# Kernel tuning notes

Hardware: AMD Instinct MI355X
Metric: run time of the kernel (lower is better)

## Reference

```python
import jax, jax.numpy as jnp
import numpy as np

ALPHA = 1.0  # set_privacy(True)


def setup_inputs() -> dict:
    key = jax.random.key(0)
    k1, k2, k3, k4, k5, k6 = jax.random.split(key, 6)
    B, S, IN, OUT = 2, 1024, 4096, 11008
    NNZ = 2250000
    x = jax.random.normal(k1, (B, S, IN), dtype=jnp.float32)
    scales = jax.random.uniform(k2, (OUT,), dtype=jnp.float32)  # positive per-row scales
    ortho_vals = jax.random.normal(k3, (NNZ,), dtype=jnp.float32)
    base_packed = jax.random.randint(k4, (OUT, IN // 2), 0, 256, dtype=jnp.int32)
    ortho_rows = jnp.sort(jax.random.randint(k5, (NNZ,), 0, OUT, dtype=jnp.int32))
    ortho_cols = jax.random.randint(k6, (NNZ,), 0, IN, dtype=jnp.int32)
    return {"x": x, "scales": scales, "ortho_vals": ortho_vals,
            "base_packed": base_packed, "ortho_rows": ortho_rows, "ortho_cols": ortho_cols}


def _dequant_weight(base_packed, scales):
    OUT, HALF = base_packed.shape
    low = base_packed & 0xF          # packed column 2j  -> original column 2j
    high = (base_packed >> 4) & 0xF  # packed column 2j  -> original column 2j+1
    # interleave low/high nibbles back to [OUT, IN]
    w_off = jnp.stack([low, high], axis=-1).reshape(OUT, 2 * HALF)
    return (w_off.astype(jnp.float32) - 8.0) * scales[:, None]


def reference(x, scales, ortho_vals, base_packed, ortho_rows, ortho_cols):
    OUT = base_packed.shape[0]
    IN = base_packed.shape[1] * 2
    w_base = _dequant_weight(base_packed, scales)  # [OUT, IN] fp32
    w_sparse = jnp.zeros((OUT, IN), dtype=jnp.float32).at[ortho_rows, ortho_cols].add(
        ortho_vals.astype(jnp.float32))
    w = w_base + ALPHA * w_sparse
    x_flat = x.reshape(-1, IN).astype(jnp.float32)
    out = x_flat @ w.T  # [tokens, OUT]
    return out.reshape(x.shape[:-1] + (OUT,)).astype(x.dtype)
```

## Files before the change

kernel.cpp:

```cpp
#include <hip/hip_runtime.h>
#include <stdint.h>

#define ALPHA 1.0f

typedef int i32x4 __attribute__((ext_vector_type(4)));

typedef __attribute__((address_space(3))) void lds_void_t;
typedef const __attribute__((address_space(1))) void global_void_t;

__device__ __forceinline__ void async16(const void* g, void* l) {
    __builtin_amdgcn_global_load_lds((global_void_t*)g, (lds_void_t*)l, 16, 0, 0);
}

__device__ __forceinline__ signed char q8(float v, float inv) {
    float f = fminf(fmaxf(v * inv, -127.f), 127.f);
    return (signed char)__float2int_rn(f);
}

__global__ __launch_bounds__(256) void prep_kernel(
    const float* __restrict__ x, const int* __restrict__ rows,
    int* __restrict__ rstart, int* __restrict__ rend,
    signed char* __restrict__ X8, float* __restrict__ sx, int M, int nnz) {
    const int b = blockIdx.x;
    if (b < M) {
        __shared__ float red[4];
        const int t = threadIdx.x;
        const float4* xr = (const float4*)(x + (size_t)b * 4096);
        float4 v[4];
        float mx = 0.f;
#pragma unroll
        for (int i = 0; i < 4; i++) {
            v[i] = xr[t * 4 + i];
            mx = fmaxf(mx, fmaxf(fmaxf(fabsf(v[i].x), fabsf(v[i].y)),
                                 fmaxf(fabsf(v[i].z), fabsf(v[i].w))));
        }
#pragma unroll
        for (int o = 32; o > 0; o >>= 1) mx = fmaxf(mx, __shfl_xor(mx, o));
        if ((t & 63) == 0) red[t >> 6] = mx;
        __syncthreads();
        mx = fmaxf(fmaxf(red[0], red[1]), fmaxf(red[2], red[3]));
        mx = fmaxf(mx, 1e-20f);
        if (t == 0) sx[b] = mx / 127.f;
        const float inv = 127.f / mx;
        union { signed char c[16]; int4 w; } u;
#pragma unroll
        for (int i = 0; i < 4; i++) {
            u.c[i * 4 + 0] = q8(v[i].x, inv);
            u.c[i * 4 + 1] = q8(v[i].y, inv);
            u.c[i * 4 + 2] = q8(v[i].z, inv);
            u.c[i * 4 + 3] = q8(v[i].w, inv);
        }
        ((int4*)(X8 + (size_t)b * 4096))[t] = u.w;
    } else {
        int i = (b - M) * 256 + threadIdx.x;
        if (i < nnz) {
            int r = rows[i];
            if (i == 0 || rows[i - 1] != r) rstart[r] = i;
            if (i == nnz - 1 || rows[i + 1] != r) rend[r] = i + 1;
        }
    }
}

__global__ __launch_bounds__(256) void build_w8_kernel(
    const int* __restrict__ packed, const float* __restrict__ scales,
    const float* __restrict__ vals, const int* __restrict__ cols,
    const int* __restrict__ rstart, const int* __restrict__ rend,
    signed char* __restrict__ W8, float* __restrict__ sw) {
    __shared__ float acc[4096];
    __shared__ float red[4];
    const int r = blockIdx.x;
    const int t = threadIdx.x;
    const int4* prow = (const int4*)(packed + (size_t)r * 2048);
    const float s = scales[r];

    int4 p0 = prow[t], p1 = prow[t + 256];
#pragma unroll
    for (int h = 0; h < 2; h++) {
        int4 p = h ? p1 : p0;
        int base = 8 * (t + 256 * h);
        int pv[4] = {p.x, p.y, p.z, p.w};
#pragma unroll
        for (int q = 0; q < 4; q++) {
            acc[base + 2 * q]     = (float)((pv[q] & 0xF) - 8) * s;
            acc[base + 2 * q + 1] = (float)(((pv[q] >> 4) & 0xF) - 8) * s;
        }
    }
    __syncthreads();

    const int lo = rstart[r], hi = rend[r];
    for (int i = lo + t; i < hi; i += 256)
        atomicAdd(&acc[cols[i]], vals[i] * ALPHA);
    __syncthreads();

    float4 f[4];
    float mx = 0.f;
#pragma unroll
    for (int i = 0; i < 4; i++) {
        f[i] = ((const float4*)acc)[t * 4 + i];
        mx = fmaxf(mx, fmaxf(fmaxf(fabsf(f[i].x), fabsf(f[i].y)),
                             fmaxf(fabsf(f[i].z), fabsf(f[i].w))));
    }
#pragma unroll
    for (int o = 32; o > 0; o >>= 1) mx = fmaxf(mx, __shfl_xor(mx, o));
    if ((t & 63) == 0) red[t >> 6] = mx;
    __syncthreads();
    mx = fmaxf(fmaxf(red[0], red[1]), fmaxf(red[2], red[3]));
    mx = fmaxf(mx, 1e-20f);
    if (t == 0) sw[r] = mx / 127.f;
    const float inv = 127.f / mx;

    union { signed char c[16]; int4 w; } u;
#pragma unroll
    for (int i = 0; i < 4; i++) {
        u.c[i * 4 + 0] = q8(f[i].x, inv);
        u.c[i * 4 + 1] = q8(f[i].y, inv);
        u.c[i * 4 + 2] = q8(f[i].z, inv);
        u.c[i * 4 + 3] = q8(f[i].w, inv);
    }
    ((int4*)(W8 + (size_t)r * 4096))[t] = u.w;
}

__global__ __launch_bounds__(512) void gemm_kernel(
    const signed char* __restrict__ Xq,
    const signed char* __restrict__ Wq,
    const float* __restrict__ sx,
    const float* __restrict__ sw,
    float* __restrict__ C,
    int M, int N, int K) {
    __shared__ __align__(16) signed char smem[3 * 49152];

    const int tid  = threadIdx.x;
    const int wid  = tid >> 6;
    const int lane = tid & 63;
    const int wr = wid >> 2;
    const int wc = wid & 3;

    const int nwg = gridDim.x;
    const int bid = blockIdx.x;
    const int qc = nwg >> 3, rr = nwg & 7;
    const int xcd = bid & 7, loc = bid >> 3;
    const int swz = (xcd < rr ? xcd * (qc + 1) : rr * (qc + 1) + (xcd - rr) * qc) + loc;
    const int tm = M >> 7;
    const int mt = swz % tm;
    const int nt = swz / tm;
    const int m0 = mt << 7;
    const int n0 = nt << 8;

    const int sr = tid >> 3;
    const int sc = ((tid & 7) ^ (sr & 7)) << 4;
    const int lw0 = wid << 10;
    const int lw1 = 8192 + (wid << 10);

    const signed char* Ax  = Xq + (size_t)m0 * K;
    const signed char* Bw0 = Wq + (size_t)n0 * K;
    const signed char* Bw1 = Wq + (size_t)(n0 + 128) * K;

#define STAGE(gbase, ldsbase) do {                                         \
        async16((gbase) + (size_t)sr * K + sc, (ldsbase) + lw0);           \
        async16((gbase) + (size_t)(sr + 64) * K + sc, (ldsbase) + lw1);    \
    } while (0)

    const int fm = lane & 15;
    const int slot0 = ((lane >> 4) ^ (lane & 7)) << 4;
    const int slot1 = slot0 ^ 64;
    const int arow_base = wr * 64;
    const int brow_base = wc * 64;

#define LDA(buf, mi, sl) \
    (*(const i32x4*)((buf) + (size_t)(arow_base + (mi) * 16 + fm) * 128 + (sl)))
#define LDB(buf, nj, sl) \
    (*(const i32x4*)((buf) + 16384 + (size_t)(brow_base + (nj) * 16 + fm) * 128 + (sl)))

#define MFMA8(m0i, m1i, aX, aY, B0, B1, B2, B3) do {                        \
        __builtin_amdgcn_s_setprio(1);                                      \
        acc[m0i][0] = __builtin_amdgcn_mfma_i32_16x16x64_i8(aX, B0, acc[m0i][0], 0, 0, 0); \
        acc[m1i][0] = __builtin_amdgcn_mfma_i32_16x16x64_i8(aY, B0, acc[m1i][0], 0, 0, 0); \
        acc[m0i][1] = __builtin_amdgcn_mfma_i32_16x16x64_i8(aX, B1, acc[m0i][1], 0, 0, 0); \
        acc[m1i][1] = __builtin_amdgcn_mfma_i32_16x16x64_i8(aY, B1, acc[m1i][1], 0, 0, 0); \
        acc[m0i][2] = __builtin_amdgcn_mfma_i32_16x16x64_i8(aX, B2, acc[m0i][2], 0, 0, 0); \
        acc[m1i][2] = __builtin_amdgcn_mfma_i32_16x16x64_i8(aY, B2, acc[m1i][2], 0, 0, 0); \
        acc[m0i][3] = __builtin_amdgcn_mfma_i32_16x16x64_i8(aX, B3, acc[m0i][3], 0, 0, 0); \
        acc[m1i][3] = __builtin_amdgcn_mfma_i32_16x16x64_i8(aY, B3, acc[m1i][3], 0, 0, 0); \
        __builtin_amdgcn_s_setprio(0);                                      \
    } while (0)

    i32x4 acc[4][4];
#pragma unroll
    for (int i = 0; i < 4; i++)
#pragma unroll
        for (int j = 0; j < 4; j++) acc[i][j] = (i32x4){0, 0, 0, 0};

    const int NT = K >> 7;

    STAGE(Ax,        smem);
    STAGE(Bw0,       smem + 16384);
    STAGE(Bw1,       smem + 32768);
    STAGE(Ax  + 128, smem + 49152);
    STAGE(Bw0 + 128, smem + 49152 + 16384);
    STAGE(Bw1 + 128, smem + 49152 + 32768);
    asm volatile("s_waitcnt vmcnt(6)" ::: "memory");
    __builtin_amdgcn_s_barrier();
    __builtin_amdgcn_sched_barrier(0);

    int cur = 0;
    for (int it = 0; it < NT; ++it) {
        signed char* Ab = smem + cur * 49152;
        int pb = cur + 2; if (pb >= 3) pb -= 3;
        signed char* PA = smem + pb * 49152;
        const bool pref = (it + 2 < NT);
        const int kc = (it + 2) << 7;

        i32x4 a0  = LDA(Ab, 0, slot0), a1  = LDA(Ab, 1, slot0);
        i32x4 bA0 = LDB(Ab, 0, slot0), bA1 = LDB(Ab, 1, slot0),
              bA2 = LDB(Ab, 2, slot0), bA3 = LDB(Ab, 3, slot0);
        i32x4 na0 = LDA(Ab, 2, slot0), na1 = LDA(Ab, 3, slot0);
        if (pref) STAGE(Ax + kc, PA);
        MFMA8(0, 1, a0, a1, bA0, bA1, bA2, bA3);

        i32x4 bB0 = LDB(Ab, 0, slot1), bB1 = LDB(Ab, 1, slot1),
              bB2 = LDB(Ab, 2, slot1), bB3 = LDB(Ab, 3, slot1);
        i32x4 ma0 = LDA(Ab, 0, slot1), ma1 = LDA(Ab, 1, slot1);
        if (pref) STAGE(Bw0 + kc, PA + 16384);
        MFMA8(2, 3, na0, na1, bA0, bA1, bA2, bA3);

        i32x4 pa2 = LDA(Ab, 2, slot1), pa3 = LDA(Ab, 3, slot1);
        if (pref) STAGE(Bw1 + kc, PA + 32768);
        MFMA8(0, 1, ma0, ma1, bB0, bB1, bB2, bB3);

        if (it + 2 < NT)       { asm volatile("s_waitcnt vmcnt(6)" ::: "memory"); }
        else if (it + 2 == NT) { asm volatile("s_waitcnt vmcnt(0)" ::: "memory"); }
        MFMA8(2, 3, pa2, pa3, bB0, bB1, bB2, bB3);

        __builtin_amdgcn_s_barrier();
        __builtin_amdgcn_sched_barrier(0);
        cur += 1; if (cur == 3) cur = 0;
    }
#undef STAGE
#undef LDA
#undef LDB
#undef MFMA8

    const int cr = (lane >> 4) << 2;
    const int cc = lane & 15;
#pragma unroll
    for (int mi = 0; mi < 4; ++mi) {
        const int row0 = m0 + wr * 64 + mi * 16 + cr;
        float sxv[4];
#pragma unroll
        for (int r = 0; r < 4; ++r) sxv[r] = sx[row0 + r];
#pragma unroll
        for (int nj = 0; nj < 4; ++nj) {
            const int col = n0 + wc * 64 + nj * 16 + cc;
            const float swc = sw[col];
            float* cp = C + (size_t)row0 * N + col;
#pragma unroll
            for (int r = 0; r < 4; ++r)
                cp[(size_t)r * N] = (float)acc[mi][nj][r] * sxv[r] * swc;
        }
    }
}

extern "C" void kernel_launch(void* const* d_in, const int* in_sizes, int n_in,
                              void* d_out, int out_size, void* d_ws, size_t ws_size,
                              hipStream_t stream) {
    const float* x      = (const float*)d_in[0];
    const float* scales = (const float*)d_in[1];
    const float* vals   = (const float*)d_in[2];
    const int* packed   = (const int*)d_in[3];
    const int* rows     = (const int*)d_in[4];
    const int* cols     = (const int*)d_in[5];
    float* out          = (float*)d_out;

    const int OUT  = in_sizes[1];
    const int HALF = in_sizes[3] / OUT;
    const int IN   = HALF * 2;
    const int M    = in_sizes[0] / IN;
    const int NNZ  = in_sizes[2];

    signed char* W8 = (signed char*)d_ws;
    signed char* X8 = W8 + (size_t)OUT * IN;
    float* sx   = (float*)(X8 + (size_t)M * IN);
    float* sw   = sx + M;
    int* rstart = (int*)(sw + OUT);
    int* rend   = rstart + OUT;

    const int boundsBlocks = (NNZ + 255) / 256;
    prep_kernel<<<M + boundsBlocks, 256, 0, stream>>>(x, rows, rstart, rend,
                                                      X8, sx, M, NNZ);
    build_w8_kernel<<<OUT, 256, 0, stream>>>(packed, scales, vals, cols,
                                             rstart, rend, W8, sw);
    const int nwg = (M / 128) * (OUT / 256);
    gemm_kernel<<<nwg, 512, 0, stream>>>(X8, W8, sx, sw, out, M, OUT, IN);
}
```

Before: 314.0 us.

## Shrink GEMM tile to 128x128 with 256 threads and double-buffered LDS

Reworks the int8 GEMM from a 128x256 tile with 8 waves and a triple-buffered LDS pipeline (prefetch two ahead) into a 128x128 tile with 4 waves and a double-buffered pipeline (prefetch one ahead). Launch bounds now request two blocks per CU, and the smaller LDS footprint makes that possible, so the aim is more occupancy and latency hiding across blocks. In exchange there is less operand reuse per tile, the grid doubles, and each iteration waits on vmcnt(0) before its barrier, which may expose global load latency. OUT=11008 divides by 128 evenly, so coverage is preserved.

```diff
diff --git a/kernel.cpp b/kernel.cpp
--- a/kernel.cpp
+++ b/kernel.cpp
@@ -120,20 +120,20 @@
     ((int4*)(W8 + (size_t)r * 4096))[t] = u.w;
 }
 
-__global__ __launch_bounds__(512) void gemm_kernel(
+__global__ __launch_bounds__(256, 2) void gemm_kernel(
     const signed char* __restrict__ Xq,
     const signed char* __restrict__ Wq,
     const float* __restrict__ sx,
     const float* __restrict__ sw,
     float* __restrict__ C,
     int M, int N, int K) {
-    __shared__ __align__(16) signed char smem[3 * 49152];
+    __shared__ __align__(16) signed char smem[2 * 32768];
 
     const int tid  = threadIdx.x;
     const int wid  = tid >> 6;
     const int lane = tid & 63;
-    const int wr = wid >> 2;
-    const int wc = wid & 3;
+    const int wr = wid >> 1;
+    const int wc = wid & 1;
 
     const int nwg = gridDim.x;
     const int bid = blockIdx.x;
@@ -144,20 +144,23 @@
     const int mt = swz % tm;
     const int nt = swz / tm;
     const int m0 = mt << 7;
-    const int n0 = nt << 8;
+    const int n0 = nt << 7;
 
     const int sr = tid >> 3;
     const int sc = ((tid & 7) ^ (sr & 7)) << 4;
-    const int lw0 = wid << 10;
-    const int lw1 = 8192 + (wid << 10);
-
-    const signed char* Ax  = Xq + (size_t)m0 * K;
-    const signed char* Bw0 = Wq + (size_t)n0 * K;
-    const signed char* Bw1 = Wq + (size_t)(n0 + 128) * K;
-
-#define STAGE(gbase, ldsbase) do {                                         \
-        async16((gbase) + (size_t)sr * K + sc, (ldsbase) + lw0);           \
-        async16((gbase) + (size_t)(sr + 64) * K + sc, (ldsbase) + lw1);    \
+    const int lw = wid << 10;
+
+    const signed char* Ax = Xq + (size_t)m0 * K;
+    const signed char* Bw = Wq + (size_t)n0 * K;
+
+#define STAGE(abase, bbase, ldsbase) do {                                    \
+        _Pragma("unroll")                                                    \
+        for (int i_ = 0; i_ < 4; i_++) {                                     \
+            async16((abase) + (size_t)(i_ * 32 + sr) * K + sc,               \
+                    (ldsbase) + i_ * 4096 + lw);                             \
+            async16((bbase) + (size_t)(i_ * 32 + sr) * K + sc,               \
+                    (ldsbase) + 16384 + i_ * 4096 + lw);                     \
+        }                                                                    \
     } while (0)
 
     const int fm = lane & 15;
@@ -192,48 +195,35 @@
 
     const int NT = K >> 7;
 
-    STAGE(Ax,        smem);
-    STAGE(Bw0,       smem + 16384);
-    STAGE(Bw1,       smem + 32768);
-    STAGE(Ax  + 128, smem + 49152);
-    STAGE(Bw0 + 128, smem + 49152 + 16384);
-    STAGE(Bw1 + 128, smem + 49152 + 32768);
-    asm volatile("s_waitcnt vmcnt(6)" ::: "memory");
+    STAGE(Ax, Bw, smem);
+    asm volatile("s_waitcnt vmcnt(0)" ::: "memory");
     __builtin_amdgcn_s_barrier();
     __builtin_amdgcn_sched_barrier(0);
 
-    int cur = 0;
     for (int it = 0; it < NT; ++it) {
-        signed char* Ab = smem + cur * 49152;
-        int pb = cur + 2; if (pb >= 3) pb -= 3;
-        signed char* PA = smem + pb * 49152;
-        const bool pref = (it + 2 < NT);
-        const int kc = (it + 2) << 7;
+        signed char* Ab = smem + ((it & 1) << 15);
+        signed char* Pb = smem + (((it + 1) & 1) << 15);
+        const int kc = (it + 1) << 7;
 
         i32x4 a0  = LDA(Ab, 0, slot0), a1  = LDA(Ab, 1, slot0);
         i32x4 bA0 = LDB(Ab, 0, slot0), bA1 = LDB(Ab, 1, slot0),
               bA2 = LDB(Ab, 2, slot0), bA3 = LDB(Ab, 3, slot0);
         i32x4 na0 = LDA(Ab, 2, slot0), na1 = LDA(Ab, 3, slot0);
-        if (pref) STAGE(Ax + kc, PA);
+        if (it + 1 < NT) STAGE(Ax + kc, Bw + kc, Pb);
         MFMA8(0, 1, a0, a1, bA0, bA1, bA2, bA3);
 
         i32x4 bB0 = LDB(Ab, 0, slot1), bB1 = LDB(Ab, 1, slot1),
               bB2 = LDB(Ab, 2, slot1), bB3 = LDB(Ab, 3, slot1);
         i32x4 ma0 = LDA(Ab, 0, slot1), ma1 = LDA(Ab, 1, slot1);
-        if (pref) STAGE(Bw0 + kc, PA + 16384);
         MFMA8(2, 3, na0, na1, bA0, bA1, bA2, bA3);
 
         i32x4 pa2 = LDA(Ab, 2, slot1), pa3 = LDA(Ab, 3, slot1);
-        if (pref) STAGE(Bw1 + kc, PA + 32768);
         MFMA8(0, 1, ma0, ma1, bB0, bB1, bB2, bB3);
 
-        if (it + 2 < NT)       { asm volatile("s_waitcnt vmcnt(6)" ::: "memory"); }
-        else if (it + 2 == NT) { asm volatile("s_waitcnt vmcnt(0)" ::: "memory"); }
         MFMA8(2, 3, pa2, pa3, bB0, bB1, bB2, bB3);
-
+        asm volatile("s_waitcnt vmcnt(0)" ::: "memory");
         __builtin_amdgcn_s_barrier();
         __builtin_amdgcn_sched_barrier(0);
-        cur += 1; if (cur == 3) cur = 0;
     }
 #undef STAGE
 #undef LDA
@@ -289,6 +279,6 @@
                                                       X8, sx, M, NNZ);
     build_w8_kernel<<<OUT, 256, 0, stream>>>(packed, scales, vals, cols,
                                              rstart, rend, W8, sw);
-    const int nwg = (M / 128) * (OUT / 256);
-    gemm_kernel<<<nwg, 512, 0, stream>>>(X8, W8, sx, sw, out, M, OUT, IN);
-}
+    const int nwg = (M / 128) * (OUT / 128);
+    gemm_kernel<<<nwg, 256, 0, stream>>>(X8, W8, sx, sw, out, M, OUT, IN);
+}
```

New measurement: 315.2 us. About the same (+0.4%).
